# Kernel tuning notes

Hardware: AMD Instinct MI355X
Metric: run time of the kernel (lower is better)

## Reference

```python
import jax, jax.numpy as jnp
import numpy as np


def setup_inputs() -> dict:
    key = jax.random.key(0)
    k1, k2 = jax.random.split(key)
    B, D = 65536, 256
    L, K = 4, 2048
    residual = jax.random.normal(k1, (B, D), dtype=jnp.float32)
    # matches nn.Parameter(torch.randn(K, D) * 0.1) per level, stacked over L
    codebooks = jax.random.normal(k2, (L, K, D), dtype=jnp.float32) * 0.1
    return {"residual": residual, "codebooks": codebooks}


def reference(residual, codebooks):
    """Residual vector quantization over L sequential levels.

    residual:  [B, D]
    codebooks: [L, K, D]
    Returns (quantized [B, D], codes [B, L] int32).
    """
    def step(carry, emb):
        res, qsum = carry                                   # [B,D], [B,D]
        x2 = jnp.sum(res * res, axis=1, keepdims=True)      # [B,1]
        e2 = jnp.sum(emb * emb, axis=1)                     # [K]
        scores = x2 + e2 - 2.0 * (res @ emb.T)              # [B,K]
        idx = jnp.argmin(scores, axis=1)                    # [B]
        q = emb[idx]                                        # [B,D] gather
        return (res - q, qsum + q), idx

    init = (residual, jnp.zeros_like(residual))
    (_, quantized), codes = jax.lax.scan(step, init, codebooks)
    codes = jnp.transpose(codes)                            # [L,B] -> [B,L]
    return quantized, codes
```

## Files before the change

### kernel.cpp

```cpp
#include <hip/hip_runtime.h>
#include <stdint.h>

#define NB 65536
#define ND 256
#define NK 2048
#define NL 4
#define THRM 0.012f

typedef _Float16 v8h __attribute__((ext_vector_type(8)));
typedef __attribute__((ext_vector_type(4))) float v4f;
typedef unsigned long long ull;

__global__ void k_zero(int* __restrict__ cnt) {
    if (threadIdx.x < NL) cnt[threadIdx.x] = 0;
}

__global__ void k_e2(const float* __restrict__ cb, float* __restrict__ e2,
                     float* __restrict__ e2n) {
    __shared__ float tile[32 * 260];
    const int rowbase = blockIdx.x * 32;
    const float4* cb4 = (const float4*)(cb + (size_t)rowbase * ND);
    for (int it = 0; it < 32; ++it) {
        float4 v = cb4[it * 64 + threadIdx.x];
        *(float4*)&tile[it * 260 + threadIdx.x * 4] = v;
    }
    __syncthreads();
    if (threadIdx.x < 32) {
        const float* a = &tile[threadIdx.x * 260];
        float halves[2];
        for (int h = 0; h < 2; ++h) {
            const float* p = a + h * 128;
            float r8[8];
            #pragma unroll
            for (int j = 0; j < 8; ++j) r8[j] = __fmul_rn(p[j], p[j]);
            for (int i = 8; i < 128; i += 8) {
                #pragma unroll
                for (int j = 0; j < 8; ++j) r8[j] = __fadd_rn(r8[j], __fmul_rn(p[i + j], p[i + j]));
            }
            halves[h] = __fadd_rn(__fadd_rn(__fadd_rn(r8[0], r8[1]), __fadd_rn(r8[2], r8[3])),
                                  __fadd_rn(__fadd_rn(r8[4], r8[5]), __fadd_rn(r8[6], r8[7])));
        }
        const float s = __fadd_rn(halves[0], halves[1]);
        e2[rowbase + threadIdx.x] = s;
        e2n[rowbase + threadIdx.x] = -0.5f * s;
    }
}

__global__ void k_split16(const float* __restrict__ cb, unsigned short* __restrict__ ehf) {
    const int f = blockIdx.x * 256 + threadIdx.x;
    const int g = f & 31;
    const int k = (f >> 5) & (NK - 1);
    const int l = f >> 16;
    const float* p = cb + ((size_t)(l * NK + k) * ND + g * 8);
    float4 a = *(const float4*)p;
    float4 b = *(const float4*)(p + 4);
    v8h h;
    h[0] = (_Float16)a.x; h[1] = (_Float16)a.y; h[2] = (_Float16)a.z; h[3] = (_Float16)a.w;
    h[4] = (_Float16)b.x; h[5] = (_Float16)b.y; h[6] = (_Float16)b.z; h[7] = (_Float16)b.w;
    const size_t u = (size_t)(k >> 4) * 512 + (g >> 2) * 64 + (g & 3) * 16 + (k & 15);
    *(v8h*)(void*)(ehf + (size_t)l * (NK * ND) + u * 8) = h;
}

__global__ __launch_bounds__(256)
void k_res16(const float* __restrict__ residual,
             const float* __restrict__ cb,
             const int* __restrict__ idx_hist,
             unsigned short* __restrict__ resh,
             int level)
{
    const int fid = blockIdx.x * 256 + threadIdx.x;
    const int lane = fid & 63;
    const int dc = (fid >> 6) & 7;
    const int r16 = fid >> 9;
    const int row = r16 * 16 + (lane & 15);
    const int d0 = dc * 32 + (lane >> 4) * 8;
    const float* rp = residual + (size_t)row * ND + d0;
    float buf[8];
    *(float4*)&buf[0] = *(const float4*)rp;
    *(float4*)&buf[4] = *(const float4*)(rp + 4);
    for (int j = 0; j < level; ++j) {
        const int kp = idx_hist[j * NB + row];
        const float* qp = cb + ((size_t)(j * NK + kp) * ND + d0);
        #pragma unroll
        for (int c = 0; c < 8; ++c) buf[c] = __fsub_rn(buf[c], qp[c]);
    }
    v8h h;
    #pragma unroll
    for (int c = 0; c < 8; ++c) h[c] = (_Float16)buf[c];
    *(v8h*)(void*)(resh + (size_t)fid * 8) = h;
}

__device__ __forceinline__ void stage16k(const char* gbase, char* lbase, int w, int lane) {
    #pragma unroll
    for (int i = 0; i < 4; ++i)
        __builtin_amdgcn_global_load_lds(
            (const __attribute__((address_space(1))) void*)(gbase + i * 4096 + w * 1024 + lane * 16),
            (__attribute__((address_space(3))) void*)(lbase + i * 4096 + w * 1024),
            16, 0, 0);
}

__global__ __launch_bounds__(256)
void k_passA(const unsigned short* __restrict__ resh,
             const unsigned short* __restrict__ ehf,
             const float* __restrict__ e2n,
             float* __restrict__ pb1,
             int* __restrict__ pk1,
             float* __restrict__ ps2)
{
    __shared__ unsigned short btile[2][8192];
    __shared__ float e2t[512];

    const int tid = threadIdx.x;
    const int w = tid >> 6;
    const int lane = tid & 63;
    const int kloc = lane & 15;
    const int quad = lane >> 4;

    const int j = blockIdx.x;
    const int xcd = j & 7;
    const int within = j >> 3;
    const int quarter = within & 3;
    const int rowtile = xcd * 64 + (within >> 2);
    const int rowbase = rowtile * 128 + w * 32;
    const int r16 = rowbase >> 4;

    const char* src = (const char*)(const void*)(ehf + (size_t)quarter * (512 * ND));

    stage16k(src,         (char*)&btile[0][0], w, lane);
    stage16k(src + 16384, (char*)&btile[1][0], w, lane);

    v8h ah[2][8];
    const v8h* rhp = (const v8h*)(const void*)resh;
    #pragma unroll
    for (int m = 0; m < 2; ++m) {
        #pragma unroll
        for (int dc = 0; dc < 8; ++dc)
            ah[m][dc] = rhp[((size_t)(r16 + m) * 8 + dc) * 64 + lane];
    }

    e2t[tid] = e2n[quarter * 512 + tid];
    e2t[256 + tid] = e2n[quarter * 512 + 256 + tid];

    float m1[8], m2[8];
    int k1[8];
    #pragma unroll
    for (int s = 0; s < 8; ++s) { m1[s] = -3.0e38f; m2[s] = -3.0e38f; k1[s] = 0; }

    __syncthreads();

    #pragma unroll 1
    for (int kt = 0; kt < 16; ++kt) {
        const int b = kt & 1;
        #pragma unroll
        for (int nt = 0; nt < 2; ++nt) {
            const int klq = kt * 32 + nt * 16 + kloc;
            const float e2h = e2t[klq];
            const v4f cinit = {e2h, e2h, e2h, e2h};
            v4f a0a, a1a;
            v4f a0b = {0.f, 0.f, 0.f, 0.f}, a1b = {0.f, 0.f, 0.f, 0.f};
            {
                const v8h bh = *(const v8h*)(const void*)&btile[b][((nt * 8 + 0) * 64 + quad * 16 + kloc) * 8];
                a0a = __builtin_amdgcn_mfma_f32_16x16x32_f16(ah[0][0], bh, cinit, 0, 0, 0);
                a1a = __builtin_amdgcn_mfma_f32_16x16x32_f16(ah[1][0], bh, cinit, 0, 0, 0);
            }
            #pragma unroll
            for (int dc = 1; dc < 4; ++dc) {
                const v8h bh = *(const v8h*)(const void*)&btile[b][((nt * 8 + dc) * 64 + quad * 16 + kloc) * 8];
                a0a = __builtin_amdgcn_mfma_f32_16x16x32_f16(ah[0][dc], bh, a0a, 0, 0, 0);
                a1a = __builtin_amdgcn_mfma_f32_16x16x32_f16(ah[1][dc], bh, a1a, 0, 0, 0);
            }
            #pragma unroll
            for (int dc = 4; dc < 8; ++dc) {
                const v8h bh = *(const v8h*)(const void*)&btile[b][((nt * 8 + dc) * 64 + quad * 16 + kloc) * 8];
                a0b = __builtin_amdgcn_mfma_f32_16x16x32_f16(ah[0][dc], bh, a0b, 0, 0, 0);
                a1b = __builtin_amdgcn_mfma_f32_16x16x32_f16(ah[1][dc], bh, a1b, 0, 0, 0);
            }
            const int kglob = quarter * 512 + klq;
            #pragma unroll
            for (int reg = 0; reg < 4; ++reg) {
                const float v0 = a0a[reg] + a0b[reg];
                const bool g0 = v0 > m1[reg];
                m2[reg] = __builtin_amdgcn_fmed3f(v0, m1[reg], m2[reg]);
                m1[reg] = fmaxf(m1[reg], v0);
                k1[reg] = g0 ? kglob : k1[reg];
                const float v1 = a1a[reg] + a1b[reg];
                const bool g1 = v1 > m1[4 + reg];
                m2[4 + reg] = __builtin_amdgcn_fmed3f(v1, m1[4 + reg], m2[4 + reg]);
                m1[4 + reg] = fmaxf(m1[4 + reg], v1);
                k1[4 + reg] = g1 ? kglob : k1[4 + reg];
            }
        }
        __syncthreads();
        if (kt + 2 < 16)
            stage16k(src + (size_t)(kt + 2) * 16384, (char*)&btile[b][0], w, lane);
    }

    #pragma unroll
    for (int off = 1; off < 16; off <<= 1) {
        #pragma unroll
        for (int s = 0; s < 8; ++s) {
            const float o1 = __shfl_xor(m1[s], off, 16);
            const float o2 = __shfl_xor(m2[s], off, 16);
            const int   ok = __shfl_xor(k1[s], off, 16);
            const float lo = fminf(m1[s], o1);
            m2[s] = fmaxf(fmaxf(m2[s], o2), lo);
            k1[s] = (o1 > m1[s]) ? ok : k1[s];
            m1[s] = fmaxf(m1[s], o1);
        }
    }
    if (kloc == 0) {
        #pragma unroll
        for (int s = 0; s < 8; ++s) {
            const int m = s >> 2, reg = s & 3;
            const int row = rowbase + m * 16 + quad * 4 + reg;
            pb1[(size_t)quarter * NB + row] = -2.0f * m1[s];
            pk1[(size_t)quarter * NB + row] = k1[s];
            ps2[(size_t)quarter * NB + row] = -2.0f * m2[s];
        }
    }
}

__global__ void k_margin(const float* __restrict__ pb1, const int* __restrict__ pk1,
                         const float* __restrict__ ps2,
                         int* __restrict__ idx_l, float* __restrict__ codes,
                         int* __restrict__ ulist, int* __restrict__ cnt, int level)
{
    const int row = blockIdx.x * 256 + threadIdx.x;
    float b1 = pb1[row];
    int   k  = pk1[row];
    float b2 = ps2[row];
    #pragma unroll
    for (int p = 1; p < 4; ++p) {
        const float c1 = pb1[(size_t)p * NB + row];
        const float c2 = ps2[(size_t)p * NB + row];
        const int   ck = pk1[(size_t)p * NB + row];
        if (c1 < b1) { b2 = fminf(b1, c2); b1 = c1; k = ck; }
        else         { b2 = fminf(b2, c1); }
    }
    idx_l[row] = k;
    codes[(size_t)row * NL + level] = (float)k;
    if (b2 - b1 <= THRM) {
        int p = atomicAdd(cnt, 1);
        ulist[p] = row;
    }
}

__global__ __launch_bounds__(256)
void k_rr1(const float* __restrict__ residual,
           const float* __restrict__ cb,
           const float* __restrict__ emb,
           const float* __restrict__ e2,
           const int* __restrict__ idx_hist,
           const int* __restrict__ ulist,
           const int* __restrict__ cnt,
           ull* __restrict__ partial,
           int level)
{
    __shared__ float embL[64 * 260];
    __shared__ float resL[16 * 260];
    __shared__ float x2s[16];
    __shared__ int   urows[16];
    __shared__ ull   redM[16][17];

    const int t = threadIdx.x;
    const int ks = blockIdx.x & 31;
    const int rt0 = blockIdx.x >> 5;
    const int n = *cnt;
    const int nrt = (n + 15) >> 4;
    if (rt0 >= nrt) return;

    #pragma unroll
    for (int i = 0; i < 16; ++i) {
        const int fi = t + 256 * i;
        const int r = fi >> 6, q = fi & 63;
        *(float4*)&embL[r * 260 + q * 4] = *(const float4*)&emb[(size_t)(ks * 64 + r) * ND + q * 4];
    }
    const int row = t & 15;
    const int kg = t >> 4;
    float e2r[4];
    #pragma unroll
    for (int j = 0; j < 4; ++j) e2r[j] = e2[ks * 64 + kg * 4 + j];

    for (int rt = rt0; rt < nrt; rt += 64) {
        __syncthreads();
        if (t < 16) {
            const int i = rt * 16 + t;
            urows[t] = ulist[(i < n) ? i : rt * 16];
        }
        __syncthreads();
        #pragma unroll
        for (int i = 0; i < 4; ++i) {
            const int fi = t + 256 * i;
            const int r = fi >> 6, q = fi & 63;
            const int ur = urows[r];
            float4 v = ((const float4*)residual)[(size_t)ur * 64 + q];
            for (int j = 0; j < level; ++j) {
                const int kp = idx_hist[j * NB + ur];
                const float4 qv = ((const float4*)cb)[(size_t)(j * NK + kp) * 64 + q];
                v.x = __fsub_rn(v.x, qv.x);
                v.y = __fsub_rn(v.y, qv.y);
                v.z = __fsub_rn(v.z, qv.z);
                v.w = __fsub_rn(v.w, qv.w);
            }
            *(float4*)&resL[r * 260 + q * 4] = v;
        }
        __syncthreads();
        if (t < 16) {
            const float* a = &resL[t * 260];
            float halves[2];
            for (int h = 0; h < 2; ++h) {
                const float* p = a + h * 128;
                float r8[8];
                #pragma unroll
                for (int j = 0; j < 8; ++j) r8[j] = __fmul_rn(p[j], p[j]);
                for (int i = 8; i < 128; i += 8) {
                    #pragma unroll
                    for (int j = 0; j < 8; ++j) r8[j] = __fadd_rn(r8[j], __fmul_rn(p[i + j], p[i + j]));
                }
                halves[h] = __fadd_rn(__fadd_rn(__fadd_rn(r8[0], r8[1]), __fadd_rn(r8[2], r8[3])),
                                      __fadd_rn(__fadd_rn(r8[4], r8[5]), __fadd_rn(r8[6], r8[7])));
            }
            x2s[t] = __fadd_rn(halves[0], halves[1]);
        }
        __syncthreads();

        float d0 = 0.f, d1 = 0.f, d2 = 0.f, d3 = 0.f;
        const float* rp = &resL[row * 260];
        const float* ep = &embL[(kg * 4) * 260];
        #pragma unroll 8
        for (int q = 0; q < 64; ++q) {
            const float4 rv = *(const float4*)&rp[q * 4];
            const float4 e0 = *(const float4*)&ep[q * 4];
            const float4 e1 = *(const float4*)&ep[260 + q * 4];
            const float4 ee2 = *(const float4*)&ep[520 + q * 4];
            const float4 e3 = *(const float4*)&ep[780 + q * 4];
            d0 = __fmaf_rn(rv.x, e0.x, d0); d0 = __fmaf_rn(rv.y, e0.y, d0);
            d0 = __fmaf_rn(rv.z, e0.z, d0); d0 = __fmaf_rn(rv.w, e0.w, d0);
            d1 = __fmaf_rn(rv.x, e1.x, d1); d1 = __fmaf_rn(rv.y, e1.y, d1);
            d1 = __fmaf_rn(rv.z, e1.z, d1); d1 = __fmaf_rn(rv.w, e1.w, d1);
            d2 = __fmaf_rn(rv.x, ee2.x, d2); d2 = __fmaf_rn(rv.y, ee2.y, d2);
            d2 = __fmaf_rn(rv.z, ee2.z, d2); d2 = __fmaf_rn(rv.w, ee2.w, d2);
            d3 = __fmaf_rn(rv.x, e3.x, d3); d3 = __fmaf_rn(rv.y, e3.y, d3);
            d3 = __fmaf_rn(rv.z, e3.z, d3); d3 = __fmaf_rn(rv.w, e3.w, d3);
        }

        const float x2v = x2s[row];
        const int kb = ks * 64 + kg * 4;
        float s;
        ull best, u;
        s = __fsub_rn(__fadd_rn(x2v, e2r[0]), __fmul_rn(2.0f, d0));
        best = ((ull)__float_as_uint(s) << 32) | (ull)(kb + 0);
        s = __fsub_rn(__fadd_rn(x2v, e2r[1]), __fmul_rn(2.0f, d1));
        u = ((ull)__float_as_uint(s) << 32) | (ull)(kb + 1);
        if (u < best) best = u;
        s = __fsub_rn(__fadd_rn(x2v, e2r[2]), __fmul_rn(2.0f, d2));
        u = ((ull)__float_as_uint(s) << 32) | (ull)(kb + 2);
        if (u < best) best = u;
        s = __fsub_rn(__fadd_rn(x2v, e2r[3]), __fmul_rn(2.0f, d3));
        u = ((ull)__float_as_uint(s) << 32) | (ull)(kb + 3);
        if (u < best) best = u;

        redM[row][kg] = best;
        __syncthreads();
        if (t < 16) {
            ull b = redM[t][0];
            #pragma unroll
            for (int g = 1; g < 16; ++g) { const ull v = redM[t][g]; if (v < b) b = v; }
            partial[(size_t)(rt * 16 + t) * 32 + ks] = b;
        }
    }
}

__global__ void k_rr2(const ull* __restrict__ partial,
                      const int* __restrict__ ulist,
                      const int* __restrict__ cnt,
                      int* __restrict__ idx_l,
                      float* __restrict__ codes,
                      int level)
{
    const int n = *cnt;
    for (int i = blockIdx.x * 256 + threadIdx.x; i < n; i += gridDim.x * 256) {
        const ull* p = &partial[(size_t)i * 32];
        ull b = p[0];
        #pragma unroll
        for (int s2 = 1; s2 < 32; ++s2) { const ull v = p[s2]; if (v < b) b = v; }
        const int k = (int)(b & 0xffffffffull);
        const int row = ulist[i];
        idx_l[row] = k;
        codes[(size_t)row * NL + level] = (float)k;
    }
}

__global__ void k_finalize(const float* __restrict__ cb, const int* __restrict__ idx_hist,
                           float4* __restrict__ outq) {
    const int i = blockIdx.x * 256 + threadIdx.x;
    const int r = i >> 6, c = i & 63;
    const float4* cb4 = (const float4*)cb;
    const int i0 = idx_hist[r];
    const int i1 = idx_hist[NB + r];
    const int i2 = idx_hist[2 * NB + r];
    const int i3 = idx_hist[3 * NB + r];
    float4 q = cb4[(size_t)i0 * 64 + c];
    float4 t1 = cb4[(size_t)(NK + i1) * 64 + c];
    q.x = __fadd_rn(q.x, t1.x); q.y = __fadd_rn(q.y, t1.y);
    q.z = __fadd_rn(q.z, t1.z); q.w = __fadd_rn(q.w, t1.w);
    float4 t2 = cb4[(size_t)(2 * NK + i2) * 64 + c];
    q.x = __fadd_rn(q.x, t2.x); q.y = __fadd_rn(q.y, t2.y);
    q.z = __fadd_rn(q.z, t2.z); q.w = __fadd_rn(q.w, t2.w);
    float4 t3 = cb4[(size_t)(3 * NK + i3) * 64 + c];
    q.x = __fadd_rn(q.x, t3.x); q.y = __fadd_rn(q.y, t3.y);
    q.z = __fadd_rn(q.z, t3.z); q.w = __fadd_rn(q.w, t3.w);
    outq[i] = q;
}

extern "C" void kernel_launch(void* const* d_in, const int* in_sizes, int n_in,
                              void* d_out, int out_size, void* d_ws, size_t ws_size,
                              hipStream_t stream) {
    const float* residual = (const float*)d_in[0];
    const float* cb = (const float*)d_in[1];

    float* pb1 = (float*)d_ws;
    int* pk1 = (int*)(pb1 + 4 * (size_t)NB);
    float* ps2 = (float*)(pk1 + 4 * (size_t)NB);
    ull* partial = (ull*)(ps2 + 4 * (size_t)NB);
    float* e2 = (float*)(partial + (size_t)(NB + 16) * 32);
    float* e2n = e2 + (size_t)NL * NK;
    int* idx_hist = (int*)(e2n + (size_t)NL * NK);
    int* ulist = idx_hist + (size_t)NL * NB;
    int* cnt = ulist + NB;
    unsigned short* ehf = (unsigned short*)(cnt + 64);
    unsigned short* resh = ehf + (size_t)NL * NK * ND;

    float* codes = (float*)d_out + (size_t)NB * ND;

    k_zero<<<1, 64, 0, stream>>>(cnt);
    k_e2<<<NL * NK / 32, 64, 0, stream>>>(cb, e2, e2n);
    k_split16<<<NL * NK * 32 / 256, 256, 0, stream>>>(cb, ehf);

    for (int l = 0; l < NL; ++l) {
        const unsigned short* ehl = ehf + (size_t)l * NK * ND;
        const float* e2l = e2 + (size_t)l * NK;
        const float* e2nl = e2n + (size_t)l * NK;
        int* idx_l = idx_hist + (size_t)l * NB;
        k_res16<<<NB * ND / 8 / 256, 256, 0, stream>>>(residual, cb, idx_hist, resh, l);
        k_passA<<<NB / 128 * 4, 256, 0, stream>>>(resh, ehl, e2nl, pb1, pk1, ps2);
        k_margin<<<NB / 256, 256, 0, stream>>>(pb1, pk1, ps2, idx_l, codes, ulist, cnt + l, l);
        k_rr1<<<2048, 256, 0, stream>>>(residual, cb, cb + (size_t)l * NK * ND, e2l,
                                        idx_hist, ulist, cnt + l, partial, l);
        k_rr2<<<64, 256, 0, stream>>>(partial, ulist, cnt + l, idx_l, codes, l);
    }
    k_finalize<<<NB * ND / 4 / 256, 256, 0, stream>>>(cb, idx_hist, (float4*)d_out);
}
```

Before: 940.6 us.

## Read codebook from global in refine kernel and parallelize row norm

The refinement kernel no longer stages a 64-row codebook slice into LDS (about 66KB). Each thread instead reads its four codebook rows straight from global/L2 memory, which lowers LDS use and should raise occupancy. The row-norm computation now uses all 256 threads with shuffle reductions rather than 16 serial threads. Unroll drops from 8 to 4. The cost is repeated uncoalesced global loads of the codebook for every row tile, and the changed summation order could alter tie results near the threshold.

```diff
diff --git a/kernel.cpp b/kernel.cpp
--- a/kernel.cpp
+++ b/kernel.cpp
@@ -256,7 +256,6 @@
            ull* __restrict__ partial,
            int level)
 {
-    __shared__ float embL[64 * 260];
     __shared__ float resL[16 * 260];
     __shared__ float x2s[16];
     __shared__ int   urows[16];
@@ -269,17 +268,12 @@
     const int nrt = (n + 15) >> 4;
     if (rt0 >= nrt) return;
 
-    #pragma unroll
-    for (int i = 0; i < 16; ++i) {
-        const int fi = t + 256 * i;
-        const int r = fi >> 6, q = fi & 63;
-        *(float4*)&embL[r * 260 + q * 4] = *(const float4*)&emb[(size_t)(ks * 64 + r) * ND + q * 4];
-    }
     const int row = t & 15;
     const int kg = t >> 4;
     float e2r[4];
     #pragma unroll
     for (int j = 0; j < 4; ++j) e2r[j] = e2[ks * 64 + kg * 4 + j];
+    const float* ep = emb + (size_t)(ks * 64 + kg * 4) * ND;
 
     for (int rt = rt0; rt < nrt; rt += 64) {
         __syncthreads();
@@ -305,35 +299,31 @@
             *(float4*)&resL[r * 260 + q * 4] = v;
         }
         __syncthreads();
-        if (t < 16) {
-            const float* a = &resL[t * 260];
-            float halves[2];
-            for (int h = 0; h < 2; ++h) {
-                const float* p = a + h * 128;
-                float r8[8];
-                #pragma unroll
-                for (int j = 0; j < 8; ++j) r8[j] = __fmul_rn(p[j], p[j]);
-                for (int i = 8; i < 128; i += 8) {
-                    #pragma unroll
-                    for (int j = 0; j < 8; ++j) r8[j] = __fadd_rn(r8[j], __fmul_rn(p[i + j], p[i + j]));
-                }
-                halves[h] = __fadd_rn(__fadd_rn(__fadd_rn(r8[0], r8[1]), __fadd_rn(r8[2], r8[3])),
-                                      __fadd_rn(__fadd_rn(r8[4], r8[5]), __fadd_rn(r8[6], r8[7])));
-            }
-            x2s[t] = __fadd_rn(halves[0], halves[1]);
+        {
+            const int xr = t >> 4;
+            const int h = (t >> 3) & 1;
+            const int jj = t & 7;
+            const float* p = &resL[xr * 260 + h * 128];
+            float v = __fmul_rn(p[jj], p[jj]);
+            for (int i = 8; i < 128; i += 8)
+                v = __fadd_rn(v, __fmul_rn(p[i + jj], p[i + jj]));
+            v = __fadd_rn(v, __shfl_xor(v, 1, 16));
+            v = __fadd_rn(v, __shfl_xor(v, 2, 16));
+            v = __fadd_rn(v, __shfl_xor(v, 4, 16));
+            v = __fadd_rn(v, __shfl_xor(v, 8, 16));
+            if ((t & 15) == 0) x2s[xr] = v;
         }
         __syncthreads();
 
         float d0 = 0.f, d1 = 0.f, d2 = 0.f, d3 = 0.f;
         const float* rp = &resL[row * 260];
-        const float* ep = &embL[(kg * 4) * 260];
-        #pragma unroll 8
+        #pragma unroll 4
         for (int q = 0; q < 64; ++q) {
             const float4 rv = *(const float4*)&rp[q * 4];
             const float4 e0 = *(const float4*)&ep[q * 4];
-            const float4 e1 = *(const float4*)&ep[260 + q * 4];
-            const float4 ee2 = *(const float4*)&ep[520 + q * 4];
-            const float4 e3 = *(const float4*)&ep[780 + q * 4];
+            const float4 e1 = *(const float4*)&ep[ND + q * 4];
+            const float4 ee2 = *(const float4*)&ep[2 * ND + q * 4];
+            const float4 e3 = *(const float4*)&ep[3 * ND + q * 4];
             d0 = __fmaf_rn(rv.x, e0.x, d0); d0 = __fmaf_rn(rv.y, e0.y, d0);
             d0 = __fmaf_rn(rv.z, e0.z, d0); d0 = __fmaf_rn(rv.w, e0.w, d0);
             d1 = __fmaf_rn(rv.x, e1.x, d1); d1 = __fmaf_rn(rv.y, e1.y, d1);
```

Result: faster. 904.6 us (-3.8%).
